# Kernel tuning notes

Hardware: AMD Instinct MI355X
Metric: run time of the kernel (lower is better)

Reference implementation:

```python
import jax, jax.numpy as jnp
import numpy as np


def setup_inputs() -> dict:
    key = jax.random.key(0)
    ks = jax.random.split(key, 9)
    B, T, C, H = 4, 2048, 1024, 16
    hd = C // H  # 64
    s = 0.02
    return {
        "x": jax.random.normal(ks[0], (B, T, C), dtype=jnp.float32),
        "Wq": jax.random.normal(ks[1], (H, C, hd), dtype=jnp.float32) * s,
        "bq": jax.random.normal(ks[2], (H, hd), dtype=jnp.float32) * s,
        "Wk": jax.random.normal(ks[3], (H, C, hd), dtype=jnp.float32) * s,
        "bk": jax.random.normal(ks[4], (H, hd), dtype=jnp.float32) * s,
        "Wv": jax.random.normal(ks[5], (H, C, hd), dtype=jnp.float32) * s,
        "bv": jax.random.normal(ks[6], (H, hd), dtype=jnp.float32) * s,
        "Wp": jax.random.normal(ks[7], (C, C), dtype=jnp.float32) * s,
        "bp": jax.random.normal(ks[8], (C,), dtype=jnp.float32) * s,
    }


def reference(x, Wq, bq, Wk, bk, Wv, bv, Wp, bp):
    B, T, C = x.shape
    # per-head projections, batched over heads: [B,H,T,hd]
    q = jnp.einsum('btc,hcd->bhtd', x, Wq) + bq[None, :, None, :]
    k = jnp.einsum('btc,hcd->bhtd', x, Wk) + bk[None, :, None, :]
    v = jnp.einsum('btc,hcd->bhtd', x, Wv) + bv[None, :, None, :]
    # NOTE: original scales by full embed dim C (not head_size) -- faithful quirk
    scale = jnp.asarray(C, x.dtype) ** -0.5
    wei = jnp.einsum('bhtd,bhsd->bhts', q, k) * scale  # [B,H,T,T]
    causal = jnp.tril(jnp.ones((T, T), dtype=bool))
    wei = jnp.where(causal, wei, jnp.asarray(-jnp.inf, wei.dtype))
    wei = jax.nn.softmax(wei, axis=-1)
    out = jnp.einsum('bhts,bhsd->bhtd', wei, v)  # [B,H,T,hd]
    # concat heads along feature dim -> [B,T,C]
    out = out.transpose(0, 2, 1, 3).reshape(B, T, C)
    return out @ Wp + bp
```

## Files before the change

### kernel.cpp

```cpp
#include <hip/hip_runtime.h>
#include <hip/hip_bf16.h>
#include <stdint.h>


typedef unsigned short u16;
typedef __attribute__((ext_vector_type(4))) float f32x4;
typedef __attribute__((ext_vector_type(8))) __bf16 bf16x8;
typedef __attribute__((ext_vector_type(2))) __bf16 bf16x2;

#define DEV static __device__ __forceinline__

DEV u16 f2bf(float f) {
  uint32_t u = __builtin_bit_cast(uint32_t, f);
  return (u16)((u + 0x7FFFu + ((u >> 16) & 1u)) >> 16);
}

DEV uint pack2(float a, float b) {
  bf16x2 v;
  v.x = (__bf16)a;
  v.y = (__bf16)b;
  return __builtin_bit_cast(uint, v);
}

#if __has_builtin(__builtin_amdgcn_exp2f)
DEV float fexp2(float x) { return __builtin_amdgcn_exp2f(x); }
#else
DEV float fexp2(float x) { return __expf(x * 0.69314718056f); }
#endif

DEV void gload_lds16(const void* g, void* lds) {
  auto gp = reinterpret_cast<const __attribute__((address_space(1))) uint32_t*>(
      reinterpret_cast<uintptr_t>(g));
  auto lp = reinterpret_cast<__attribute__((address_space(3))) uint32_t*>(
      static_cast<uint32_t>(reinterpret_cast<uintptr_t>(lds)));
  __builtin_amdgcn_global_load_lds(gp, lp, 16, 0, 0);
}

DEV f32x4 mfma16(bf16x8 a, bf16x8 b, f32x4 c) {
  return __builtin_amdgcn_mfma_f32_16x16x32_bf16(a, b, c, 0, 0, 0);
}

DEV void bar() {
  asm volatile("" ::: "memory");
  __builtin_amdgcn_s_barrier();
  asm volatile("" ::: "memory");
}

#define LD8(p) (*reinterpret_cast<const bf16x8*>(p))
#define LDU4(p) (*reinterpret_cast<const uint4*>(p))


__global__ void cvt_x_kernel(const float* __restrict__ x, u16* __restrict__ xb, int n8) {
  int i = blockIdx.x * blockDim.x + threadIdx.x;
  int stride = gridDim.x * blockDim.x;
  for (; i < n8; i += stride) {
    const float4* xp = reinterpret_cast<const float4*>(x) + 2 * (size_t)i;
    float4 a = xp[0], b = xp[1];
    uint4 o;
    o.x = pack2(a.x, a.y);
    o.y = pack2(a.z, a.w);
    o.z = pack2(b.x, b.y);
    o.w = pack2(b.z, b.w);
    reinterpret_cast<uint4*>(xb)[i] = o;
  }
}

__global__ void cvt_wqkv_kernel(const float* __restrict__ Wq, const float* __restrict__ Wk,
                                const float* __restrict__ Wv, const float* __restrict__ bq,
                                const float* __restrict__ bk, const float* __restrict__ bv,
                                u16* __restrict__ wt, float* __restrict__ biasq) {
  __shared__ u16 tle[64 * 72];
  const int tid = threadIdx.x;
  const int ct = blockIdx.x;
  const int h = blockIdx.y;
  const int which = blockIdx.z;
  const float* W = (which == 0) ? Wq : (which == 1) ? Wk : Wv;
  const float* Bb = (which == 0) ? bq : (which == 1) ? bk : bv;
  const float scl = (which == 0) ? 0.045084220027780106f : 1.0f;
#pragma unroll
  for (int i = 0; i < 4; ++i) {
    int idx = i * 256 + tid;
    int c_l = idx >> 4, d4 = (idx & 15) * 4;
    float4 v = *reinterpret_cast<const float4*>(&W[((size_t)(h * 1024 + ct * 64 + c_l)) * 64 + d4]);
    tle[(d4 + 0) * 72 + c_l] = f2bf(v.x * scl);
    tle[(d4 + 1) * 72 + c_l] = f2bf(v.y * scl);
    tle[(d4 + 2) * 72 + c_l] = f2bf(v.z * scl);
    tle[(d4 + 3) * 72 + c_l] = f2bf(v.w * scl);
  }
  __syncthreads();
#pragma unroll
  for (int i = 0; i < 2; ++i) {
    int idx = i * 256 + tid;
    int d_o = idx >> 3, c8 = (idx & 7) * 8;
    uint4 v = LDU4(&tle[d_o * 72 + c8]);
    *reinterpret_cast<uint4*>(&wt[(size_t)(which * 1024 + h * 64 + d_o) * 1024 + ct * 64 + c8]) = v;
  }
  if (ct == 0 && tid < 64) biasq[which * 1024 + h * 64 + tid] = Bb[h * 64 + tid] * scl;
}

__global__ void cvt_wp_kernel(const float* __restrict__ Wp, u16* __restrict__ wpt) {
  __shared__ u16 tle[64 * 72];
  const int tid = threadIdx.x;
  const int ct = blockIdx.x;
  const int nt = blockIdx.y;
#pragma unroll
  for (int i = 0; i < 4; ++i) {
    int idx = i * 256 + tid;
    int c_l = idx >> 4, n4 = (idx & 15) * 4;
    float4 v = *reinterpret_cast<const float4*>(&Wp[(size_t)(ct * 64 + c_l) * 1024 + nt * 64 + n4]);
    tle[(n4 + 0) * 72 + c_l] = f2bf(v.x);
    tle[(n4 + 1) * 72 + c_l] = f2bf(v.y);
    tle[(n4 + 2) * 72 + c_l] = f2bf(v.z);
    tle[(n4 + 3) * 72 + c_l] = f2bf(v.w);
  }
  __syncthreads();
#pragma unroll
  for (int i = 0; i < 2; ++i) {
    int idx = i * 256 + tid;
    int n_o = idx >> 3, c8 = (idx & 7) * 8;
    uint4 v = LDU4(&tle[n_o * 72 + c8]);
    *reinterpret_cast<uint4*>(&wpt[(size_t)(nt * 64 + n_o) * 1024 + ct * 64 + c8]) = v;
  }
}

__global__ __launch_bounds__(256)
void transpose_v_kernel(const u16* __restrict__ qkv, u16* __restrict__ vT) {
  __shared__ alignas(16) u16 tle[64 * 72];
  const int tid = threadIdx.x;
  const int tt = blockIdx.x;
  const int h = blockIdx.y;
  const int bb = blockIdx.z;
  const size_t rbase = ((size_t)bb * 2048 + tt * 64) * 3072 + 2048 + h * 64;
#pragma unroll
  for (int i = 0; i < 2; ++i) {
    int idx = i * 256 + tid;
    int s = idx >> 3, c8 = (idx & 7) * 8;
    *reinterpret_cast<uint4*>(&tle[s * 72 + c8]) = LDU4(&qkv[rbase + (size_t)s * 3072 + c8]);
  }
  __syncthreads();
#pragma unroll
  for (int i = 0; i < 2; ++i) {
    int idx = i * 256 + tid;
    int d = idx >> 3, cb = idx & 7;
    uint4 o;
    o.x = (uint)tle[(2 * cb + 0) * 72 + d] | ((uint)tle[(16 + 2 * cb + 0) * 72 + d] << 16);
    o.y = (uint)tle[(32 + 2 * cb + 0) * 72 + d] | ((uint)tle[(48 + 2 * cb + 0) * 72 + d] << 16);
    o.z = (uint)tle[(2 * cb + 1) * 72 + d] | ((uint)tle[(16 + 2 * cb + 1) * 72 + d] << 16);
    o.w = (uint)tle[(32 + 2 * cb + 1) * 72 + d] | ((uint)tle[(48 + 2 * cb + 1) * 72 + d] << 16);
    *reinterpret_cast<uint4*>(
        &vT[((size_t)(bb * 16 + h) * 64 + d) * 2048 + tt * 64 + cb * 8]) = o;
  }
}


template <bool OUT_F32>
__global__ __launch_bounds__(512, 4)
void gemm13_kernel(const u16* __restrict__ A, const u16* __restrict__ Bt,
                   const float* __restrict__ bias, void* __restrict__ Cout,
                   int M, int N, int K, int nbn) {
  __shared__ alignas(16) u16 LA[2 * 4096];
  __shared__ alignas(16) u16 LB[2 * 8192];

  const int tid = threadIdx.x;
  const int lane = tid & 63;
  const int wave = tid >> 6;
  const int wm = wave >> 2;
  const int wn = wave & 3;
  const int fr = lane & 15;
  const int kg = lane >> 4;
  const int r4 = kg * 4;

  const int nwg = gridDim.x;
  const int swz = (blockIdx.x & 7) * (nwg >> 3) + (blockIdx.x >> 3);
  const int m0 = (swz / nbn) * 128;
  const int n0 = (swz % nbn) * 256;
  const int NT = K >> 5;

  const int srow = tid >> 2;
  const int sgcol = (((tid & 3) ^ ((srow >> 1) & 3)) << 3);
  const size_t aOff = (size_t)(m0 + srow) * K + sgcol;
  const size_t bOff = (size_t)(n0 + srow) * K + sgcol;
  const int ldst = tid * 8;

  auto stageA = [&](int kt, u16* d) {
    gload_lds16(A + aOff + (size_t)kt * 32, d + ldst);
  };
  auto stageB = [&](int kt, u16* d) {
    gload_lds16(Bt + bOff + (size_t)kt * 32, d + ldst);
    gload_lds16(Bt + bOff + (size_t)128 * K + (size_t)kt * 32, d + 4096 + ldst);
  };

  f32x4 acc[4][4] = {};

  stageA(0, LA);
  stageB(0, LB);
  asm volatile("s_waitcnt vmcnt(0)" ::: "memory");
  bar();

  for (int kt = 0; kt < NT; ++kt) {
    const bool st1 = (kt + 1 < NT);
    u16* la = LA + (kt & 1) * 4096;
    u16* lb = LB + (kt & 1) * 8192;

    if (st1) {
      stageA(kt + 1, LA + ((kt + 1) & 1) * 4096);
      stageB(kt + 1, LB + ((kt + 1) & 1) * 8192);
    }

    bf16x8 aF[4], bF[4];
#pragma unroll
    for (int m = 0; m < 4; ++m) {
      const int R = wm * 64 + m * 16 + fr;
      aF[m] = LD8(&la[R * 32 + ((kg ^ ((R >> 1) & 3)) << 3)]);
    }
#pragma unroll
    for (int n = 0; n < 4; ++n) {
      const int R = wn * 64 + n * 16 + fr;
      bF[n] = LD8(&lb[R * 32 + ((kg ^ ((R >> 1) & 3)) << 3)]);
    }

    __builtin_amdgcn_s_setprio(1);
#pragma unroll
    for (int m = 0; m < 4; ++m)
#pragma unroll
      for (int n = 0; n < 4; ++n)
        acc[m][n] = mfma16(aF[m], bF[n], acc[m][n]);
    __builtin_amdgcn_s_setprio(0);

    if (st1) {
      asm volatile("s_waitcnt vmcnt(0)" ::: "memory");
      bar();
    }
  }

#pragma unroll
  for (int m = 0; m < 4; ++m) {
    const int row = m0 + wm * 64 + m * 16 + r4;
#pragma unroll
    for (int n = 0; n < 4; ++n) {
      const int col = n0 + wn * 64 + n * 16 + fr;
      const float bv = bias[col];
#pragma unroll
      for (int r = 0; r < 4; ++r) {
        float v = acc[m][n][r] + bv;
        size_t off = (size_t)(row + r) * N + col;
        if constexpr (OUT_F32) reinterpret_cast<float*>(Cout)[off] = v;
        else                   reinterpret_cast<u16*>(Cout)[off] = f2bf(v);
      }
    }
  }
}


template <bool OUT_F32>
__global__ __launch_bounds__(512, 2)
void gemm9_kernel(const u16* __restrict__ A, const u16* __restrict__ Bt,
                  const float* __restrict__ bias, void* __restrict__ Cout,
                  int M, int N, int K, int nbn) {
  __shared__ alignas(16) u16 LA[2 * 8192];
  __shared__ alignas(16) u16 LB[3 * 16384];

  const int tid = threadIdx.x;
  const int lane = tid & 63;
  const int wave = tid >> 6;
  const int wm = wave >> 2;
  const int wn = wave & 3;
  const int fr = lane & 15;
  const int kg = lane >> 4;
  const int f7 = fr & 7;
  const int r4 = kg * 4;

  const int nwg = gridDim.x;
  const int swz = (blockIdx.x & 7) * (nwg >> 3) + (blockIdx.x >> 3);
  const int m0 = (swz / nbn) * 128;
  const int n0 = (swz % nbn) * 256;
  const int NT = K >> 6;

  const int srow = tid >> 3;
  const int sgcol = ((tid & 7) ^ (srow & 7)) << 3;
  const size_t aOff = (size_t)(m0 + srow) * K + sgcol;
  const size_t bOff = (size_t)(n0 + srow) * K + sgcol;
  const int ldst = tid * 8;

  auto stageA = [&](int kt, u16* labuf) {
    gload_lds16(A + aOff + (size_t)kt * 64, labuf + ldst);
    gload_lds16(A + aOff + (size_t)64 * K + (size_t)kt * 64, labuf + 4096 + ldst);
  };
  auto stageB = [&](int kt, u16* lbbuf) {
    gload_lds16(Bt + bOff + (size_t)kt * 64, lbbuf + ldst);
    gload_lds16(Bt + bOff + (size_t)64 * K + (size_t)kt * 64, lbbuf + 4096 + ldst);
    gload_lds16(Bt + bOff + (size_t)128 * K + (size_t)kt * 64, lbbuf + 8192 + ldst);
    gload_lds16(Bt + bOff + (size_t)192 * K + (size_t)kt * 64, lbbuf + 12288 + ldst);
  };

  f32x4 acc[4][4] = {};

  stageA(0, LA);
  stageB(0, LB);
  if (NT > 1) {
    stageB(1, LB + 16384);
    asm volatile("s_waitcnt vmcnt(4)" ::: "memory");
  } else {
    asm volatile("s_waitcnt vmcnt(0)" ::: "memory");
  }
  bar();

  for (int kt = 0; kt < NT; ++kt) {
    const bool st1 = (kt + 1 < NT);
    const bool st2 = (kt + 2 < NT);
    u16* laCur = LA + (kt & 1) * 8192;
    u16* lbCur = LB + (kt % 3) * 16384;

    if (st1) stageA(kt + 1, LA + ((kt + 1) & 1) * 8192);
    if (st2) stageB(kt + 2, LB + ((kt + 2) % 3) * 16384);

    bf16x8 aF[4][2], bF[4][2];
#pragma unroll
    for (int m = 0; m < 4; ++m)
#pragma unroll
      for (int ks = 0; ks < 2; ++ks)
        aF[m][ks] = LD8(&laCur[wm * 4096 + (m * 16 + fr) * 64 + (((ks * 4 + kg) ^ f7) << 3)]);
#pragma unroll
    for (int n = 0; n < 4; ++n)
#pragma unroll
      for (int ks = 0; ks < 2; ++ks)
        bF[n][ks] = LD8(&lbCur[wn * 4096 + (n * 16 + fr) * 64 + (((ks * 4 + kg) ^ f7) << 3)]);

    __builtin_amdgcn_s_setprio(1);
#pragma unroll
    for (int ks = 0; ks < 2; ++ks)
#pragma unroll
      for (int m = 0; m < 4; ++m)
#pragma unroll
        for (int n = 0; n < 4; ++n)
          acc[m][n] = mfma16(aF[m][ks], bF[n][ks], acc[m][n]);
    __builtin_amdgcn_s_setprio(0);

    if (st1) {
      if (st2) asm volatile("s_waitcnt vmcnt(4)" ::: "memory");
      else     asm volatile("s_waitcnt vmcnt(0)" ::: "memory");
      bar();
    }
  }

#pragma unroll
  for (int m = 0; m < 4; ++m) {
    const int row = m0 + wm * 64 + m * 16 + r4;
#pragma unroll
    for (int n = 0; n < 4; ++n) {
      const int col = n0 + wn * 64 + n * 16 + fr;
      const float bv = bias[col];
#pragma unroll
      for (int r = 0; r < 4; ++r) {
        float v = acc[m][n][r] + bv;
        size_t off = (size_t)(row + r) * N + col;
        if constexpr (OUT_F32) reinterpret_cast<float*>(Cout)[off] = v;
        else                   reinterpret_cast<u16*>(Cout)[off] = f2bf(v);
      }
    }
  }
}


__global__ __launch_bounds__(128, 2)
void attn_kernel(const u16* __restrict__ qkv, const u16* __restrict__ vT,
                 u16* __restrict__ obuf) {
  __shared__ alignas(16) u16 Ks[64 * 72];
  __shared__ alignas(16) u16 Vs[64 * 72];
  __shared__ alignas(16) u16 Ps[2][32 * 72];

  const int tid = threadIdx.x;
  const int lane = tid & 63;
  const int wave = tid >> 6;

  const int gid = blockIdx.x;
  const int xcd = gid & 7;
  const int jj = gid >> 3;
  const int g = xcd * 8 + (jj >> 4);
  const int pair = jj & 15;
  const int bb = g >> 4;
  const int h = g & 15;

  const size_t baseQ = (size_t)bb * 2048 * 3072 + h * 64;
  const size_t baseK = baseQ + 1024;
  const size_t baseVt = (size_t)(bb * 16 + h) * 64 * 2048;

  const int fr = lane & 15;
  const int kg8 = (lane >> 4) * 8;
  const int qw32 = wave * 32;
  const int r4 = (lane >> 4) * 4;

  const int rrA = tid >> 3;
  const int cA8 = (tid & 7) * 8;
  const size_t gK = (size_t)rrA * 3072 + cA8;
  const size_t gV = (size_t)rrA * 2048 + cA8;
  const int lof = rrA * 72 + cA8;
  u16* __restrict__ Pw = &Ps[wave][0];

  for (int half = 0; half < 2; ++half) {
    const int qt = half ? (31 - pair) : pair;
    const int q0 = qt * 64;
    const int nt = qt + 1;

    const u16* qrow0 = &qkv[baseQ + (size_t)(q0 + qw32 + fr) * 3072 + kg8];
    bf16x8 aq00 = LD8(qrow0), aq01 = LD8(qrow0 + 32);
    const u16* qrow1 = qrow0 + 16 * 3072;
    bf16x8 aq10 = LD8(qrow1), aq11 = LD8(qrow1 + 32);

    float lsA0 = 0.f, lsA1 = 0.f, lsA2 = 0.f, lsA3 = 0.f;
    float lsB0 = 0.f, lsB1 = 0.f, lsB2 = 0.f, lsB3 = 0.f;
    f32x4 oA0 = {}, oA1 = {}, oA2 = {}, oA3 = {};
    f32x4 oB0 = {}, oB1 = {}, oB2 = {}, oB3 = {};

    uint4 kr0 = LDU4(&qkv[baseK + gK]);
    uint4 kr1 = LDU4(&qkv[baseK + gK + 49152]);
    uint4 kr2 = LDU4(&qkv[baseK + gK + 98304]);
    uint4 kr3 = LDU4(&qkv[baseK + gK + 147456]);
    uint4 vr0 = LDU4(&vT[baseVt + gV]);
    uint4 vr1 = LDU4(&vT[baseVt + gV + 32768]);
    uint4 vr2 = LDU4(&vT[baseVt + gV + 65536]);
    uint4 vr3 = LDU4(&vT[baseVt + gV + 98304]);

    for (int t = 0; t < nt; ++t) {
      __syncthreads();
      *reinterpret_cast<uint4*>(&Ks[lof]) = kr0;
      *reinterpret_cast<uint4*>(&Ks[lof + 1152]) = kr1;
      *reinterpret_cast<uint4*>(&Ks[lof + 2304]) = kr2;
      *reinterpret_cast<uint4*>(&Ks[lof + 3456]) = kr3;
      *reinterpret_cast<uint4*>(&Vs[lof]) = vr0;
      *reinterpret_cast<uint4*>(&Vs[lof + 1152]) = vr1;
      *reinterpret_cast<uint4*>(&Vs[lof + 2304]) = vr2;
      *reinterpret_cast<uint4*>(&Vs[lof + 3456]) = vr3;
      if (t + 1 < nt) {
        const u16* nk = &qkv[baseK + (size_t)(t + 1) * 196608];
        const u16* nv = &vT[baseVt + (size_t)(t + 1) * 64];
        kr0 = LDU4(nk + gK);
        kr1 = LDU4(nk + gK + 49152);
        kr2 = LDU4(nk + gK + 98304);
        kr3 = LDU4(nk + gK + 147456);
        vr0 = LDU4(nv + gV);
        vr1 = LDU4(nv + gV + 32768);
        vr2 = LDU4(nv + gV + 65536);
        vr3 = LDU4(nv + gV + 98304);
      }
      __syncthreads();

      f32x4 sA0 = {}, sA1 = {}, sA2 = {}, sA3 = {};
      f32x4 sB0 = {}, sB1 = {}, sB2 = {}, sB3 = {};
      {
        bf16x8 b;
        __builtin_amdgcn_s_setprio(1);
        b = LD8(&Ks[(fr) * 72 + kg8]);           sA0 = mfma16(aq00, b, sA0); sB0 = mfma16(aq10, b, sB0);
        b = LD8(&Ks[(16 + fr) * 72 + kg8]);      sA1 = mfma16(aq00, b, sA1); sB1 = mfma16(aq10, b, sB1);
        b = LD8(&Ks[(32 + fr) * 72 + kg8]);      sA2 = mfma16(aq00, b, sA2); sB2 = mfma16(aq10, b, sB2);
        b = LD8(&Ks[(48 + fr) * 72 + kg8]);      sA3 = mfma16(aq00, b, sA3); sB3 = mfma16(aq10, b, sB3);
        b = LD8(&Ks[(fr) * 72 + 32 + kg8]);      sA0 = mfma16(aq01, b, sA0); sB0 = mfma16(aq11, b, sB0);
        b = LD8(&Ks[(16 + fr) * 72 + 32 + kg8]); sA1 = mfma16(aq01, b, sA1); sB1 = mfma16(aq11, b, sB1);
        b = LD8(&Ks[(32 + fr) * 72 + 32 + kg8]); sA2 = mfma16(aq01, b, sA2); sB2 = mfma16(aq11, b, sB2);
        b = LD8(&Ks[(48 + fr) * 72 + 32 + kg8]); sA3 = mfma16(aq01, b, sA3); sB3 = mfma16(aq11, b, sB3);
        __builtin_amdgcn_s_setprio(0);
      }

      const bool diag = (t == nt - 1);
#define SM_ROW_G(S0, S1, S2, S3, LS, RB, r)                                    \
      {                                                                        \
        const int qg = qw32 + RB + r4 + r;                                     \
        float p0 = fexp2(S0[r]);                                               \
        float p1 = fexp2(S1[r]);                                               \
        float p2 = fexp2(S2[r]);                                               \
        float p3 = fexp2(S3[r]);                                               \
        if (diag) {                                                            \
          if (fr > qg) p0 = 0.f;                                               \
          if (fr + 16 > qg) p1 = 0.f;                                          \
          if (fr + 32 > qg) p2 = 0.f;                                          \
          if (fr + 48 > qg) p3 = 0.f;                                          \
        }                                                                      \
        LS += (p0 + p1) + (p2 + p3);                                           \
        uint2 w;                                                               \
        w.x = pack2(p0, p1);                                                   \
        w.y = pack2(p2, p3);                                                   \
        *reinterpret_cast<uint2*>(&Pw[(RB + r4 + r) * 72 + fr * 4]) = w;       \
      }
      SM_ROW_G(sA0, sA1, sA2, sA3, lsA0, 0, 0)
      SM_ROW_G(sA0, sA1, sA2, sA3, lsA1, 0, 1)
      SM_ROW_G(sA0, sA1, sA2, sA3, lsA2, 0, 2)
      SM_ROW_G(sA0, sA1, sA2, sA3, lsA3, 0, 3)
      SM_ROW_G(sB0, sB1, sB2, sB3, lsB0, 16, 0)
      SM_ROW_G(sB0, sB1, sB2, sB3, lsB1, 16, 1)
      SM_ROW_G(sB0, sB1, sB2, sB3, lsB2, 16, 2)
      SM_ROW_G(sB0, sB1, sB2, sB3, lsB3, 16, 3)
#undef SM_ROW_G

      {
        bf16x8 pfA = LD8(&Pw[fr * 72 + kg8]);
        bf16x8 pfB = LD8(&Pw[(16 + fr) * 72 + kg8]);
        bf16x8 v;
        __builtin_amdgcn_s_setprio(1);
        v = LD8(&Vs[(fr) * 72 + kg8]);           oA0 = mfma16(pfA, v, oA0); oB0 = mfma16(pfB, v, oB0);
        v = LD8(&Vs[(16 + fr) * 72 + kg8]);      oA1 = mfma16(pfA, v, oA1); oB1 = mfma16(pfB, v, oB1);
        v = LD8(&Vs[(32 + fr) * 72 + kg8]);      oA2 = mfma16(pfA, v, oA2); oB2 = mfma16(pfB, v, oB2);
        v = LD8(&Vs[(48 + fr) * 72 + kg8]);      oA3 = mfma16(pfA, v, oA3); oB3 = mfma16(pfB, v, oB3);
        pfA = LD8(&Pw[fr * 72 + 32 + kg8]);
        pfB = LD8(&Pw[(16 + fr) * 72 + 32 + kg8]);
        v = LD8(&Vs[(fr) * 72 + 32 + kg8]);      oA0 = mfma16(pfA, v, oA0); oB0 = mfma16(pfB, v, oB0);
        v = LD8(&Vs[(16 + fr) * 72 + 32 + kg8]); oA1 = mfma16(pfA, v, oA1); oB1 = mfma16(pfB, v, oB1);
        v = LD8(&Vs[(32 + fr) * 72 + 32 + kg8]); oA2 = mfma16(pfA, v, oA2); oB2 = mfma16(pfB, v, oB2);
        v = LD8(&Vs[(48 + fr) * 72 + 32 + kg8]); oA3 = mfma16(pfA, v, oA3); oB3 = mfma16(pfB, v, oB3);
        __builtin_amdgcn_s_setprio(0);
      }
    }

#define EPI_G(O0, O1, O2, O3, LS, RB, r)                                       \
    {                                                                          \
      float s = LS;                                                            \
      s += __shfl_xor(s, 1);                                                   \
      s += __shfl_xor(s, 2);                                                   \
      s += __shfl_xor(s, 4);                                                   \
      s += __shfl_xor(s, 8);                                                   \
      const float inv = 1.0f / s;                                              \
      const int qg = q0 + qw32 + RB + r4 + r;                                  \
      const size_t rowoff = ((size_t)bb * 2048 + qg) * 1024 + h * 64;          \
      obuf[rowoff + fr] = f2bf(O0[r] * inv);                                   \
      obuf[rowoff + 16 + fr] = f2bf(O1[r] * inv);                              \
      obuf[rowoff + 32 + fr] = f2bf(O2[r] * inv);                              \
      obuf[rowoff + 48 + fr] = f2bf(O3[r] * inv);                              \
    }
    EPI_G(oA0, oA1, oA2, oA3, lsA0, 0, 0)
    EPI_G(oA0, oA1, oA2, oA3, lsA1, 0, 1)
    EPI_G(oA0, oA1, oA2, oA3, lsA2, 0, 2)
    EPI_G(oA0, oA1, oA2, oA3, lsA3, 0, 3)
    EPI_G(oB0, oB1, oB2, oB3, lsB0, 16, 0)
    EPI_G(oB0, oB1, oB2, oB3, lsB1, 16, 1)
    EPI_G(oB0, oB1, oB2, oB3, lsB2, 16, 2)
    EPI_G(oB0, oB1, oB2, oB3, lsB3, 16, 3)
#undef EPI_G
  }
}


extern "C" void kernel_launch(void* const* d_in, const int* in_sizes, int n_in,
                              void* d_out, int out_size, void* d_ws, size_t ws_size,
                              hipStream_t stream) {
  const float* x  = (const float*)d_in[0];
  const float* Wq = (const float*)d_in[1];
  const float* bq = (const float*)d_in[2];
  const float* Wk = (const float*)d_in[3];
  const float* bk = (const float*)d_in[4];
  const float* Wv = (const float*)d_in[5];
  const float* bv = (const float*)d_in[6];
  const float* Wp = (const float*)d_in[7];
  const float* bp = (const float*)d_in[8];

  char* ws = (char*)d_ws;
  size_t off = 0;
  auto alloc = [&](size_t bytes) -> void* {
    void* p = ws + off;
    off += (bytes + 255) & ~(size_t)255;
    return p;
  };
  u16*   xb     = (u16*)  alloc((size_t)8192 * 1024 * 2);
  u16*   wqkv_t = (u16*)  alloc((size_t)3072 * 1024 * 2);
  float* biasq  = (float*)alloc((size_t)3072 * 4);
  u16*   wpt    = (u16*)  alloc((size_t)1024 * 1024 * 2);
  u16*   qkv    = (u16*)  alloc((size_t)8192 * 3072 * 2);
  u16*   obuf   = (u16*)  alloc((size_t)8192 * 1024 * 2);
  u16*   vT     = xb;
  (void)ws_size; (void)in_sizes; (void)n_in; (void)out_size;

  cvt_x_kernel<<<2048, 256, 0, stream>>>(x, xb, 8192 * 1024 / 8);
  cvt_wqkv_kernel<<<dim3(16, 16, 3), 256, 0, stream>>>(Wq, Wk, Wv, bq, bk, bv, wqkv_t, biasq);
  cvt_wp_kernel<<<dim3(16, 16), 256, 0, stream>>>(Wp, wpt);
  gemm13_kernel<false><<<768, 512, 0, stream>>>(xb, wqkv_t, biasq, qkv, 8192, 3072, 1024, 12);
  transpose_v_kernel<<<dim3(32, 16, 4), 256, 0, stream>>>(qkv, vT);
  attn_kernel<<<1024, 128, 0, stream>>>(qkv, vT, obuf);
  gemm9_kernel<true><<<256, 512, 0, stream>>>(obuf, wpt, bp, d_out, 8192, 1024, 1024, 4);
}
```

Measured before the change: 158.1 us.

## Enlarge attention query tile and double-buffer K/V via direct global-to-LDS loads

The attention kernel now gives each wave 64 query rows instead of 32, so each block covers 128 queries and the grid is halved. K/V tiles are loaded straight into double-buffered LDS with XOR-swizzled layouts, replacing register staging and padded rows, which leaves one barrier per iteration. The goal is more K/V reuse per load and better overlap of loads with MFMA work. In exchange each wave holds far more accumulator registers, which can lower occupancy, and the two waves get uneven causal work on the diagonal.

```diff
diff --git a/kernel.cpp b/kernel.cpp
--- a/kernel.cpp
+++ b/kernel.cpp
@@ -362,12 +362,12 @@
 }
 
 
-__global__ __launch_bounds__(128, 2)
+__global__ __launch_bounds__(128)
 void attn_kernel(const u16* __restrict__ qkv, const u16* __restrict__ vT,
                  u16* __restrict__ obuf) {
-  __shared__ alignas(16) u16 Ks[64 * 72];
-  __shared__ alignas(16) u16 Vs[64 * 72];
-  __shared__ alignas(16) u16 Ps[2][32 * 72];
+  __shared__ alignas(16) u16 Ks[2][64 * 64];
+  __shared__ alignas(16) u16 Vs[2][64 * 64];
+  __shared__ alignas(16) u16 Ps[2][64 * 72];
 
   const int tid = threadIdx.x;
   const int lane = tid & 63;
@@ -375,9 +375,9 @@
 
   const int gid = blockIdx.x;
   const int xcd = gid & 7;
-  const int jj = gid >> 3;
-  const int g = xcd * 8 + (jj >> 4);
-  const int pair = jj & 15;
+  const int j = gid >> 3;
+  const int g = xcd * 8 + (j >> 3);
+  const int pair = j & 7;
   const int bb = g >> 4;
   const int h = g & 15;
 
@@ -386,131 +386,144 @@
   const size_t baseVt = (size_t)(bb * 16 + h) * 64 * 2048;
 
   const int fr = lane & 15;
-  const int kg8 = (lane >> 4) * 8;
-  const int qw32 = wave * 32;
-  const int r4 = (lane >> 4) * 4;
-
-  const int rrA = tid >> 3;
-  const int cA8 = (tid & 7) * 8;
-  const size_t gK = (size_t)rrA * 3072 + cA8;
-  const size_t gV = (size_t)rrA * 2048 + cA8;
-  const int lof = rrA * 72 + cA8;
+  const int kg = lane >> 4;
+  const int kg8 = kg * 8;
+  const int r4 = kg * 4;
+  const int f7 = fr & 7;
+  const int ko0 = (kg ^ f7) * 8;
+  const int ko1 = ((4 + kg) ^ f7) * 8;
   u16* __restrict__ Pw = &Ps[wave][0];
 
+  auto stageKV = [&](int t, int bi) {
+    const u16* kS = qkv + baseK + (size_t)t * 64 * 3072;
+    const u16* vS = vT + baseVt + (size_t)t * 64;
+#pragma unroll
+    for (int i = 0; i < 4; ++i) {
+      const int c = i * 128 + tid;
+      const int rr = c >> 3;
+      const int ss = ((c & 7) ^ (rr & 7)) * 8;
+      gload_lds16(kS + (size_t)rr * 3072 + ss, &Ks[bi][c * 8]);
+      gload_lds16(vS + (size_t)rr * 2048 + ss, &Vs[bi][c * 8]);
+    }
+  };
+
   for (int half = 0; half < 2; ++half) {
-    const int qt = half ? (31 - pair) : pair;
-    const int q0 = qt * 64;
-    const int nt = qt + 1;
-
-    const u16* qrow0 = &qkv[baseQ + (size_t)(q0 + qw32 + fr) * 3072 + kg8];
-    bf16x8 aq00 = LD8(qrow0), aq01 = LD8(qrow0 + 32);
-    const u16* qrow1 = qrow0 + 16 * 3072;
-    bf16x8 aq10 = LD8(qrow1), aq11 = LD8(qrow1 + 32);
-
-    float lsA0 = 0.f, lsA1 = 0.f, lsA2 = 0.f, lsA3 = 0.f;
-    float lsB0 = 0.f, lsB1 = 0.f, lsB2 = 0.f, lsB3 = 0.f;
-    f32x4 oA0 = {}, oA1 = {}, oA2 = {}, oA3 = {};
-    f32x4 oB0 = {}, oB1 = {}, oB2 = {}, oB3 = {};
-
-    uint4 kr0 = LDU4(&qkv[baseK + gK]);
-    uint4 kr1 = LDU4(&qkv[baseK + gK + 49152]);
-    uint4 kr2 = LDU4(&qkv[baseK + gK + 98304]);
-    uint4 kr3 = LDU4(&qkv[baseK + gK + 147456]);
-    uint4 vr0 = LDU4(&vT[baseVt + gV]);
-    uint4 vr1 = LDU4(&vT[baseVt + gV + 32768]);
-    uint4 vr2 = LDU4(&vT[baseVt + gV + 65536]);
-    uint4 vr3 = LDU4(&vT[baseVt + gV + 98304]);
+    const int qt = half ? (15 - pair) : pair;
+    const int q0 = qt * 128;
+    const int nt = 2 * qt + 2;
+    const int myNt = nt - 1 + wave;
+    const int qw = wave * 64;
+
+    const u16* qr = &qkv[baseQ + (size_t)(q0 + qw + fr) * 3072 + kg8];
+    bf16x8 aq00 = LD8(qr), aq01 = LD8(qr + 32);
+    bf16x8 aq10 = LD8(qr + 16 * 3072), aq11 = LD8(qr + 16 * 3072 + 32);
+    bf16x8 aq20 = LD8(qr + 32 * 3072), aq21 = LD8(qr + 32 * 3072 + 32);
+    bf16x8 aq30 = LD8(qr + 48 * 3072), aq31 = LD8(qr + 48 * 3072 + 32);
+
+    float ls00 = 0.f, ls01 = 0.f, ls02 = 0.f, ls03 = 0.f;
+    float ls10 = 0.f, ls11 = 0.f, ls12 = 0.f, ls13 = 0.f;
+    float ls20 = 0.f, ls21 = 0.f, ls22 = 0.f, ls23 = 0.f;
+    float ls30 = 0.f, ls31 = 0.f, ls32 = 0.f, ls33 = 0.f;
+    f32x4 o00 = {}, o01 = {}, o02 = {}, o03 = {};
+    f32x4 o10 = {}, o11 = {}, o12 = {}, o13 = {};
+    f32x4 o20 = {}, o21 = {}, o22 = {}, o23 = {};
+    f32x4 o30 = {}, o31 = {}, o32 = {}, o33 = {};
+
+    stageKV(0, 0);
+    asm volatile("s_waitcnt vmcnt(0)" ::: "memory");
+    bar();
 
     for (int t = 0; t < nt; ++t) {
-      __syncthreads();
-      *reinterpret_cast<uint4*>(&Ks[lof]) = kr0;
-      *reinterpret_cast<uint4*>(&Ks[lof + 1152]) = kr1;
-      *reinterpret_cast<uint4*>(&Ks[lof + 2304]) = kr2;
-      *reinterpret_cast<uint4*>(&Ks[lof + 3456]) = kr3;
-      *reinterpret_cast<uint4*>(&Vs[lof]) = vr0;
-      *reinterpret_cast<uint4*>(&Vs[lof + 1152]) = vr1;
-      *reinterpret_cast<uint4*>(&Vs[lof + 2304]) = vr2;
-      *reinterpret_cast<uint4*>(&Vs[lof + 3456]) = vr3;
-      if (t + 1 < nt) {
-        const u16* nk = &qkv[baseK + (size_t)(t + 1) * 196608];
-        const u16* nv = &vT[baseVt + (size_t)(t + 1) * 64];
-        kr0 = LDU4(nk + gK);
-        kr1 = LDU4(nk + gK + 49152);
-        kr2 = LDU4(nk + gK + 98304);
-        kr3 = LDU4(nk + gK + 147456);
-        vr0 = LDU4(nv + gV);
-        vr1 = LDU4(nv + gV + 32768);
-        vr2 = LDU4(nv + gV + 65536);
-        vr3 = LDU4(nv + gV + 98304);
+      if (t + 1 < nt) stageKV(t + 1, (t + 1) & 1);
+
+      if (t < myNt) {
+        const u16* ks = &Ks[t & 1][0];
+        const u16* vs = &Vs[t & 1][0];
+
+        f32x4 s00 = {}, s01 = {}, s02 = {}, s03 = {};
+        f32x4 s10 = {}, s11 = {}, s12 = {}, s13 = {};
+        f32x4 s20 = {}, s21 = {}, s22 = {}, s23 = {};
+        f32x4 s30 = {}, s31 = {}, s32 = {}, s33 = {};
+        {
+          bf16x8 b;
+          __builtin_amdgcn_s_setprio(1);
+          b = LD8(&ks[(fr) * 64 + ko0]);      s00 = mfma16(aq00, b, s00); s10 = mfma16(aq10, b, s10); s20 = mfma16(aq20, b, s20); s30 = mfma16(aq30, b, s30);
+          b = LD8(&ks[(16 + fr) * 64 + ko0]); s01 = mfma16(aq00, b, s01); s11 = mfma16(aq10, b, s11); s21 = mfma16(aq20, b, s21); s31 = mfma16(aq30, b, s31);
+          b = LD8(&ks[(32 + fr) * 64 + ko0]); s02 = mfma16(aq00, b, s02); s12 = mfma16(aq10, b, s12); s22 = mfma16(aq20, b, s22); s32 = mfma16(aq30, b, s32);
+          b = LD8(&ks[(48 + fr) * 64 + ko0]); s03 = mfma16(aq00, b, s03); s13 = mfma16(aq10, b, s13); s23 = mfma16(aq20, b, s23); s33 = mfma16(aq30, b, s33);
+          b = LD8(&ks[(fr) * 64 + ko1]);      s00 = mfma16(aq01, b, s00); s10 = mfma16(aq11, b, s10); s20 = mfma16(aq21, b, s20); s30 = mfma16(aq31, b, s30);
+          b = LD8(&ks[(16 + fr) * 64 + ko1]); s01 = mfma16(aq01, b, s01); s11 = mfma16(aq11, b, s11); s21 = mfma16(aq21, b, s21); s31 = mfma16(aq31, b, s31);
+          b = LD8(&ks[(32 + fr) * 64 + ko1]); s02 = mfma16(aq01, b, s02); s12 = mfma16(aq11, b, s12); s22 = mfma16(aq21, b, s22); s32 = mfma16(aq31, b, s32);
+          b = LD8(&ks[(48 + fr) * 64 + ko1]); s03 = mfma16(aq01, b, s03); s13 = mfma16(aq11, b, s13); s23 = mfma16(aq21, b, s23); s33 = mfma16(aq31, b, s33);
+          __builtin_amdgcn_s_setprio(0);
+        }
+
+        const bool diag = (t == myNt - 1);
+#define SM_ROW(G, r, Sa, Sb, Sc, Sd, LS)                                       \
+        {                                                                      \
+          const int qgl = G * 16 + r4 + r;                                     \
+          float p0 = fexp2(Sa[r]);                                             \
+          float p1 = fexp2(Sb[r]);                                             \
+          float p2 = fexp2(Sc[r]);                                             \
+          float p3 = fexp2(Sd[r]);                                             \
+          if (diag) {                                                          \
+            if (fr > qgl) p0 = 0.f;                                            \
+            if (fr + 16 > qgl) p1 = 0.f;                                       \
+            if (fr + 32 > qgl) p2 = 0.f;                                       \
+            if (fr + 48 > qgl) p3 = 0.f;                                       \
+          }                                                                    \
+          LS += (p0 + p1) + (p2 + p3);                                         \
+          uint2 w;                                                             \
+          w.x = pack2(p0, p1);                                                 \
+          w.y = pack2(p2, p3);                                                 \
+          *reinterpret_cast<uint2*>(&Pw[(G * 16 + r4 + r) * 72 + fr * 4]) = w; \
+        }
+        SM_ROW(0, 0, s00, s01, s02, s03, ls00)
+        SM_ROW(0, 1, s00, s01, s02, s03, ls01)
+        SM_ROW(0, 2, s00, s01, s02, s03, ls02)
+        SM_ROW(0, 3, s00, s01, s02, s03, ls03)
+        SM_ROW(1, 0, s10, s11, s12, s13, ls10)
+        SM_ROW(1, 1, s10, s11, s12, s13, ls11)
+        SM_ROW(1, 2, s10, s11, s12, s13, ls12)
+        SM_ROW(1, 3, s10, s11, s12, s13, ls13)
+        SM_ROW(2, 0, s20, s21, s22, s23, ls20)
+        SM_ROW(2, 1, s20, s21, s22, s23, ls21)
+        SM_ROW(2, 2, s20, s21, s22, s23, ls22)
+        SM_ROW(2, 3, s20, s21, s22, s23, ls23)
+        SM_ROW(3, 0, s30, s31, s32, s33, ls30)
+        SM_ROW(3, 1, s30, s31, s32, s33, ls31)
+        SM_ROW(3, 2, s30, s31, s32, s33, ls32)
+        SM_ROW(3, 3, s30, s31, s32, s33, ls33)
+#undef SM_ROW
+
+        {
+          bf16x8 v;
+          __builtin_amdgcn_s_setprio(1);
+          bf16x8 pf0 = LD8(&Pw[(fr) * 72 + kg8]);
+          bf16x8 pf1 = LD8(&Pw[(16 + fr) * 72 + kg8]);
+          bf16x8 pf2 = LD8(&Pw[(32 + fr) * 72 + kg8]);
+          bf16x8 pf3 = LD8(&Pw[(48 + fr) * 72 + kg8]);
+          v = LD8(&vs[(fr) * 64 + ko0]);      o00 = mfma16(pf0, v, o00); o10 = mfma16(pf1, v, o10); o20 = mfma16(pf2, v, o20); o30 = mfma16(pf3, v, o30);
+          v = LD8(&vs[(16 + fr) * 64 + ko0]); o01 = mfma16(pf0, v, o01); o11 = mfma16(pf1, v, o11); o21 = mfma16(pf2, v, o21); o31 = mfma16(pf3, v, o31);
+          v = LD8(&vs[(32 + fr) * 64 + ko0]); o02 = mfma16(pf0, v, o02); o12 = mfma16(pf1, v, o12); o22 = mfma16(pf2, v, o22); o32 = mfma16(pf3, v, o32);
+          v = LD8(&vs[(48 + fr) * 64 + ko0]); o03 = mfma16(pf0, v, o03); o13 = mfma16(pf1, v, o13); o23 = mfma16(pf2, v, o23); o33 = mfma16(pf3, v, o33);
+          pf0 = LD8(&Pw[(fr) * 72 + 32 + kg8]);
+          pf1 = LD8(&Pw[(16 + fr) * 72 + 32 + kg8]);
+          pf2 = LD8(&Pw[(32 + fr) * 72 + 32 + kg8]);
+          pf3 = LD8(&Pw[(48 + fr) * 72 + 32 + kg8]);
+          v = LD8(&vs[(fr) * 64 + ko1]);      o00 = mfma16(pf0, v, o00); o10 = mfma16(pf1, v, o10); o20 = mfma16(pf2, v, o20); o30 = mfma16(pf3, v, o30);
+          v = LD8(&vs[(16 + fr) * 64 + ko1]); o01 = mfma16(pf0, v, o01); o11 = mfma16(pf1, v, o11); o21 = mfma16(pf2, v, o21); o31 = mfma16(pf3, v, o31);
+          v = LD8(&vs[(32 + fr) * 64 + ko1]); o02 = mfma16(pf0, v, o02); o12 = mfma16(pf1, v, o12); o22 = mfma16(pf2, v, o22); o32 = mfma16(pf3, v, o32);
+          v = LD8(&vs[(48 + fr) * 64 + ko1]); o03 = mfma16(pf0, v, o03); o13 = mfma16(pf1, v, o13); o23 = mfma16(pf2, v, o23); o33 = mfma16(pf3, v, o33);
+          __builtin_amdgcn_s_setprio(0);
+        }
       }
-      __syncthreads();
-
-      f32x4 sA0 = {}, sA1 = {}, sA2 = {}, sA3 = {};
-      f32x4 sB0 = {}, sB1 = {}, sB2 = {}, sB3 = {};
-      {
-        bf16x8 b;
-        __builtin_amdgcn_s_setprio(1);
-        b = LD8(&Ks[(fr) * 72 + kg8]);           sA0 = mfma16(aq00, b, sA0); sB0 = mfma16(aq10, b, sB0);
-        b = LD8(&Ks[(16 + fr) * 72 + kg8]);      sA1 = mfma16(aq00, b, sA1); sB1 = mfma16(aq10, b, sB1);
-        b = LD8(&Ks[(32 + fr) * 72 + kg8]);      sA2 = mfma16(aq00, b, sA2); sB2 = mfma16(aq10, b, sB2);
-        b = LD8(&Ks[(48 + fr) * 72 + kg8]);      sA3 = mfma16(aq00, b, sA3); sB3 = mfma16(aq10, b, sB3);
-        b = LD8(&Ks[(fr) * 72 + 32 + kg8]);      sA0 = mfma16(aq01, b, sA0); sB0 = mfma16(aq11, b, sB0);
-        b = LD8(&Ks[(16 + fr) * 72 + 32 + kg8]); sA1 = mfma16(aq01, b, sA1); sB1 = mfma16(aq11, b, sB1);
-        b = LD8(&Ks[(32 + fr) * 72 + 32 + kg8]); sA2 = mfma16(aq01, b, sA2); sB2 = mfma16(aq11, b, sB2);
-        b = LD8(&Ks[(48 + fr) * 72 + 32 + kg8]); sA3 = mfma16(aq01, b, sA3); sB3 = mfma16(aq11, b, sB3);
-        __builtin_amdgcn_s_setprio(0);
-      }
-
-      const bool diag = (t == nt - 1);
-#define SM_ROW_G(S0, S1, S2, S3, LS, RB, r)                                    \
-      {                                                                        \
-        const int qg = qw32 + RB + r4 + r;                                     \
-        float p0 = fexp2(S0[r]);                                               \
-        float p1 = fexp2(S1[r]);                                               \
-        float p2 = fexp2(S2[r]);                                               \
-        float p3 = fexp2(S3[r]);                                               \
-        if (diag) {                                                            \
-          if (fr > qg) p0 = 0.f;                                               \
-          if (fr + 16 > qg) p1 = 0.f;                                          \
-          if (fr + 32 > qg) p2 = 0.f;                                          \
-          if (fr + 48 > qg) p3 = 0.f;                                          \
-        }                                                                      \
-        LS += (p0 + p1) + (p2 + p3);                                           \
-        uint2 w;                                                               \
-        w.x = pack2(p0, p1);                                                   \
-        w.y = pack2(p2, p3);                                                   \
-        *reinterpret_cast<uint2*>(&Pw[(RB + r4 + r) * 72 + fr * 4]) = w;       \
-      }
-      SM_ROW_G(sA0, sA1, sA2, sA3, lsA0, 0, 0)
-      SM_ROW_G(sA0, sA1, sA2, sA3, lsA1, 0, 1)
-      SM_ROW_G(sA0, sA1, sA2, sA3, lsA2, 0, 2)
-      SM_ROW_G(sA0, sA1, sA2, sA3, lsA3, 0, 3)
-      SM_ROW_G(sB0, sB1, sB2, sB3, lsB0, 16, 0)
-      SM_ROW_G(sB0, sB1, sB2, sB3, lsB1, 16, 1)
-      SM_ROW_G(sB0, sB1, sB2, sB3, lsB2, 16, 2)
-      SM_ROW_G(sB0, sB1, sB2, sB3, lsB3, 16, 3)
-#undef SM_ROW_G
-
-      {
-        bf16x8 pfA = LD8(&Pw[fr * 72 + kg8]);
-        bf16x8 pfB = LD8(&Pw[(16 + fr) * 72 + kg8]);
-        bf16x8 v;
-        __builtin_amdgcn_s_setprio(1);
-        v = LD8(&Vs[(fr) * 72 + kg8]);           oA0 = mfma16(pfA, v, oA0); oB0 = mfma16(pfB, v, oB0);
-        v = LD8(&Vs[(16 + fr) * 72 + kg8]);      oA1 = mfma16(pfA, v, oA1); oB1 = mfma16(pfB, v, oB1);
-        v = LD8(&Vs[(32 + fr) * 72 + kg8]);      oA2 = mfma16(pfA, v, oA2); oB2 = mfma16(pfB, v, oB2);
-        v = LD8(&Vs[(48 + fr) * 72 + kg8]);      oA3 = mfma16(pfA, v, oA3); oB3 = mfma16(pfB, v, oB3);
-        pfA = LD8(&Pw[fr * 72 + 32 + kg8]);
-        pfB = LD8(&Pw[(16 + fr) * 72 + 32 + kg8]);
-        v = LD8(&Vs[(fr) * 72 + 32 + kg8]);      oA0 = mfma16(pfA, v, oA0); oB0 = mfma16(pfB, v, oB0);
-        v = LD8(&Vs[(16 + fr) * 72 + 32 + kg8]); oA1 = mfma16(pfA, v, oA1); oB1 = mfma16(pfB, v, oB1);
-        v = LD8(&Vs[(32 + fr) * 72 + 32 + kg8]); oA2 = mfma16(pfA, v, oA2); oB2 = mfma16(pfB, v, oB2);
-        v = LD8(&Vs[(48 + fr) * 72 + 32 + kg8]); oA3 = mfma16(pfA, v, oA3); oB3 = mfma16(pfB, v, oB3);
-        __builtin_amdgcn_s_setprio(0);
-      }
-    }
-
-#define EPI_G(O0, O1, O2, O3, LS, RB, r)                                       \
+
+      if (t + 1 < nt) asm volatile("s_waitcnt vmcnt(0)" ::: "memory");
+      bar();
+    }
+
+#define EPI(G, r, O0, O1, O2, O3, LS)                                          \
     {                                                                          \
       float s = LS;                                                            \
       s += __shfl_xor(s, 1);                                                   \
@@ -518,22 +531,30 @@
       s += __shfl_xor(s, 4);                                                   \
       s += __shfl_xor(s, 8);                                                   \
       const float inv = 1.0f / s;                                              \
-      const int qg = q0 + qw32 + RB + r4 + r;                                  \
+      const int qg = q0 + qw + G * 16 + r4 + r;                                \
       const size_t rowoff = ((size_t)bb * 2048 + qg) * 1024 + h * 64;          \
       obuf[rowoff + fr] = f2bf(O0[r] * inv);                                   \
       obuf[rowoff + 16 + fr] = f2bf(O1[r] * inv);                              \
       obuf[rowoff + 32 + fr] = f2bf(O2[r] * inv);                              \
       obuf[rowoff + 48 + fr] = f2bf(O3[r] * inv);                              \
     }
-    EPI_G(oA0, oA1, oA2, oA3, lsA0, 0, 0)
-    EPI_G(oA0, oA1, oA2, oA3, lsA1, 0, 1)
-    EPI_G(oA0, oA1, oA2, oA3, lsA2, 0, 2)
-    EPI_G(oA0, oA1, oA2, oA3, lsA3, 0, 3)
-    EPI_G(oB0, oB1, oB2, oB3, lsB0, 16, 0)
-    EPI_G(oB0, oB1, oB2, oB3, lsB1, 16, 1)
-    EPI_G(oB0, oB1, oB2, oB3, lsB2, 16, 2)
-    EPI_G(oB0, oB1, oB2, oB3, lsB3, 16, 3)
-#undef EPI_G
+    EPI(0, 0, o00, o01, o02, o03, ls00)
+    EPI(0, 1, o00, o01, o02, o03, ls01)
+    EPI(0, 2, o00, o01, o02, o03, ls02)
+    EPI(0, 3, o00, o01, o02, o03, ls03)
+    EPI(1, 0, o10, o11, o12, o13, ls10)
+    EPI(1, 1, o10, o11, o12, o13, ls11)
+    EPI(1, 2, o10, o11, o12, o13, ls12)
+    EPI(1, 3, o10, o11, o12, o13, ls13)
+    EPI(2, 0, o20, o21, o22, o23, ls20)
+    EPI(2, 1, o20, o21, o22, o23, ls21)
+    EPI(2, 2, o20, o21, o22, o23, ls22)
+    EPI(2, 3, o20, o21, o22, o23, ls23)
+    EPI(3, 0, o30, o31, o32, o33, ls30)
+    EPI(3, 1, o30, o31, o32, o33, ls31)
+    EPI(3, 2, o30, o31, o32, o33, ls32)
+    EPI(3, 3, o30, o31, o32, o33, ls33)
+#undef EPI
   }
 }
 
@@ -572,6 +593,6 @@
   cvt_wp_kernel<<<dim3(16, 16), 256, 0, stream>>>(Wp, wpt);
   gemm13_kernel<false><<<768, 512, 0, stream>>>(xb, wqkv_t, biasq, qkv, 8192, 3072, 1024, 12);
   transpose_v_kernel<<<dim3(32, 16, 4), 256, 0, stream>>>(qkv, vT);
-  attn_kernel<<<1024, 128, 0, stream>>>(qkv, vT, obuf);
+  attn_kernel<<<512, 128, 0, stream>>>(qkv, vT, obuf);
   gemm9_kernel<true><<<256, 512, 0, stream>>>(obuf, wpt, bp, d_out, 8192, 1024, 1024, 4);
 }
```

Result: slower. 172.1 us (+8.8%).
